# Optimization experiments

Hardware: AMD Instinct MI355X
Metric: run time of the kernel (lower is better)

## Reference

```python
import jax, jax.numpy as jnp
import numpy as np

HEADS = 8
DIM_HEAD = 64
SCALE = DIM_HEAD ** -0.5
THRESH = 0.01


def setup_inputs() -> dict:
    key = jax.random.key(0)
    ks = jax.random.split(key, 5)
    b, n, dim = 4, 2048, 512
    inner = HEADS * DIM_HEAD  # 512
    x = jax.random.normal(ks[0], (b, n, dim), dtype=jnp.float32)
    Wqkv = jax.random.normal(ks[1], (dim, 3 * inner), dtype=jnp.float32) * (dim ** -0.5)
    bqkv = jax.random.normal(ks[2], (3 * inner,), dtype=jnp.float32) * 0.02
    Wout = jax.random.normal(ks[3], (inner, dim), dtype=jnp.float32) * (inner ** -0.5)
    bout = jax.random.normal(ks[4], (dim,), dtype=jnp.float32) * 0.02
    return {"x": x, "Wqkv": Wqkv, "bqkv": bqkv, "Wout": Wout, "bout": bout}


def reference(x, Wqkv, bqkv, Wout, bout):
    b, n, dim = x.shape
    qkv = x @ Wqkv + bqkv  # [b, n, 3*inner]
    q, k, v = jnp.split(qkv, 3, axis=-1)
    # b n (h d) -> b h n d
    split_heads = lambda t: t.reshape(b, n, HEADS, DIM_HEAD).transpose(0, 2, 1, 3)
    q, k, v = split_heads(q), split_heads(k), split_heads(v)
    dots = jnp.einsum('bhid,bhjd->bhij', q, k) * SCALE
    attn = jax.nn.softmax(dots, axis=-1)
    attn = jnp.where(attn > THRESH, attn, jnp.zeros_like(attn))
    out = jnp.einsum('bhij,bhjd->bhid', attn, v)
    out = out.transpose(0, 2, 1, 3).reshape(b, n, HEADS * DIM_HEAD)
    return out @ Wout + bout
```

## Files before the change

kernel.cpp:

```cpp
#include <hip/hip_runtime.h>

#define S_   2048
#define DM   512
#define HD   64
#define BHN  32

typedef unsigned short u16;
typedef __bf16 bf16x8 __attribute__((ext_vector_type(8)));
typedef float  f32x4  __attribute__((ext_vector_type(4)));

__device__ __forceinline__ float bf2f(u16 u) {
    union { unsigned int i; float f; } v; v.i = ((unsigned int)u) << 16; return v.f;
}
__device__ __forceinline__ u16 f2bf(float f) {
    union { float f; unsigned int i; } v; v.f = f;
    unsigned int i = v.i;
    return (u16)((i + 0x7FFFu + ((i >> 16) & 1u)) >> 16);
}
__device__ __forceinline__ void split3(float x, u16& b0, u16& b1, u16& b2) {
    b0 = f2bf(x);
    const float r0 = x - bf2f(b0);
    b1 = f2bf(r0);
    const float r1 = r0 - bf2f(b1);
    b2 = f2bf(r1);
}
__device__ __forceinline__ void split3t(float x, u16& b0, u16& b1, u16& b2) {
    union { float f; unsigned int i; } v; v.f = x;
    const unsigned int i0 = v.i & 0xFFFF0000u;
    b0 = (u16)(i0 >> 16);
    union { float f; unsigned int i; } w0c; w0c.i = i0;
    const float r0 = x - w0c.f;
    union { float f; unsigned int i; } u; u.f = r0;
    const unsigned int i1 = u.i & 0xFFFF0000u;
    b1 = (u16)(i1 >> 16);
    union { float f; unsigned int i; } w1c; w1c.i = i1;
    const float r1 = r0 - w1c.f;
    union { float f; unsigned int i; } z; z.f = r1;
    b2 = (u16)(z.i >> 16);
}

__global__ __launch_bounds__(256) void prep_split_wT(
    const float* __restrict__ W, int N, int total,
    u16* __restrict__ w0, u16* __restrict__ w1, u16* __restrict__ w2)
{
    for (int idx = blockIdx.x * 256 + threadIdx.x; idx < total; idx += gridDim.x * 256) {
        const int n = idx >> 9, k = idx & 511;
        u16 a0, a1, a2;
        split3t(W[(size_t)k * N + n], a0, a1, a2);
        w0[idx] = a0; w1[idx] = a1;
        if (w2) w2[idx] = a2;
    }
}

__global__ __launch_bounds__(256) void gemm_qkv_mfma(
    const float* __restrict__ A, const u16* __restrict__ Wt0, const u16* __restrict__ Wt1,
    const u16* __restrict__ Wt2, const float* __restrict__ bias,
    float* __restrict__ qh, float* __restrict__ kh, u16* __restrict__ vt)
{
    __shared__ __attribute__((aligned(16))) u16 As0[128 * 32], As1[128 * 32], As2[128 * 32];
    __shared__ __attribute__((aligned(16))) u16 Bs0[128 * 32], Bs1[128 * 32], Bs2[128 * 32];

    const int t  = threadIdx.x;
    const int m0 = blockIdx.y * 128, n0 = blockIdx.x * 128;
    const int w  = t >> 6, l = t & 63;
    const int wm = (w >> 1) * 64, wn = (w & 1) * 64;
    const int lr = l & 15, lq = l >> 4;

    const f32x4 zero4 = {0.f, 0.f, 0.f, 0.f};
    f32x4 acc[4][4];
#pragma unroll
    for (int i = 0; i < 4; i++)
#pragma unroll
        for (int j = 0; j < 4; j++) acc[i][j] = zero4;

    for (int k0 = 0; k0 < 512; k0 += 32) {
        __syncthreads();
#pragma unroll
        for (int i = 0; i < 4; i++) {
            const int e = t + 256 * i;
            const int r = e >> 3, c4 = (e & 7) * 4;
            const float4 f = *(const float4*)(&A[(size_t)(m0 + r) * 512 + k0 + c4]);
            const float xv[4] = {f.x, f.y, f.z, f.w};
            u16 a0[4], a1[4], a2[4];
#pragma unroll
            for (int j = 0; j < 4; j++) split3t(xv[j], a0[j], a1[j], a2[j]);
            int2 p0, p1, p2;
            p0.x = a0[0] | (a0[1] << 16); p0.y = a0[2] | (a0[3] << 16);
            p1.x = a1[0] | (a1[1] << 16); p1.y = a1[2] | (a1[3] << 16);
            p2.x = a2[0] | (a2[1] << 16); p2.y = a2[2] | (a2[3] << 16);
            *(int2*)(&As0[r * 32 + c4]) = p0;
            *(int2*)(&As1[r * 32 + c4]) = p1;
            *(int2*)(&As2[r * 32 + c4]) = p2;
        }
#pragma unroll
        for (int i = 0; i < 2; i++) {
            const int e = t + 256 * i;
            const int r = e >> 2, c0 = (e & 3) * 8;
            *(int4*)(&Bs0[r * 32 + c0]) = *(const int4*)(&Wt0[(size_t)(n0 + r) * 512 + k0 + c0]);
            *(int4*)(&Bs1[r * 32 + c0]) = *(const int4*)(&Wt1[(size_t)(n0 + r) * 512 + k0 + c0]);
            *(int4*)(&Bs2[r * 32 + c0]) = *(const int4*)(&Wt2[(size_t)(n0 + r) * 512 + k0 + c0]);
        }
        __syncthreads();

#pragma unroll
        for (int i = 0; i < 4; i++) {
            const int ao = (wm + i * 16 + lr) * 32 + lq * 8;
            const bf16x8 a0 = *(const bf16x8*)(&As0[ao]);
            const bf16x8 a1 = *(const bf16x8*)(&As1[ao]);
            const bf16x8 a2 = *(const bf16x8*)(&As2[ao]);
#pragma unroll
            for (int j = 0; j < 4; j++) {
                const int bo = (wn + j * 16 + lr) * 32 + lq * 8;
                const bf16x8 b0 = *(const bf16x8*)(&Bs0[bo]);
                const bf16x8 b1 = *(const bf16x8*)(&Bs1[bo]);
                const bf16x8 b2 = *(const bf16x8*)(&Bs2[bo]);
                f32x4 c = acc[i][j];
                c = __builtin_amdgcn_mfma_f32_16x16x32_bf16(a0, b0, c, 0, 0, 0);
                c = __builtin_amdgcn_mfma_f32_16x16x32_bf16(a0, b1, c, 0, 0, 0);
                c = __builtin_amdgcn_mfma_f32_16x16x32_bf16(a1, b0, c, 0, 0, 0);
                c = __builtin_amdgcn_mfma_f32_16x16x32_bf16(a1, b1, c, 0, 0, 0);
                c = __builtin_amdgcn_mfma_f32_16x16x32_bf16(a0, b2, c, 0, 0, 0);
                c = __builtin_amdgcn_mfma_f32_16x16x32_bf16(a2, b0, c, 0, 0, 0);
                acc[i][j] = c;
            }
        }
    }

#pragma unroll
    for (int j = 0; j < 4; j++) {
        const int n = n0 + wn + j * 16 + lr;
        const float bv = bias[n];
        const int part = n >> 9, within = n & 511;
        const int h = within >> 6, d = within & 63;
#pragma unroll
        for (int i = 0; i < 4; i++) {
#pragma unroll
            for (int r = 0; r < 4; r++) {
                const int m = m0 + wm + i * 16 + lq * 4 + r;
                const int b = m >> 11, ns = m & 2047;
                const float val = acc[i][j][r] + bv;
                if (part == 0)
                    qh[(((size_t)(b * 8 + h)) * S_ + ns) * HD + d] = val;
                else if (part == 1)
                    kh[(((size_t)(b * 8 + h)) * S_ + ns) * HD + d] = val;
                else
                    vt[(((size_t)(b * 8 + h)) * HD + d) * S_ + ns] = f2bf(val);
            }
        }
    }
}

#define LDH 72

__global__ __launch_bounds__(512) void attn_mfma128(
    const float* __restrict__ q_ws, const float* __restrict__ k_ws,
    const u16* __restrict__ vt_ws, u16* __restrict__ ao_ws)
{
    __shared__ __attribute__((aligned(16))) u16 K0s[64 * LDH], K1s[64 * LDH], K2s[64 * LDH];
    __shared__ __attribute__((aligned(16))) u16 Vs[64 * LDH];
    __shared__ __attribute__((aligned(16))) u16 Ps[8][16 * LDH];
    __shared__ float smaxL[8][32];

    const int t  = threadIdx.x;
    const int w  = t >> 6, l = t & 63;
    const int lr = l & 15, lq = l >> 4;
    const int bh = blockIdx.y, b = bh >> 3, h = bh & 7;
    const int q0 = blockIdx.x * 128;

    const float* qg  = q_ws + ((size_t)bh * S_ + q0) * HD;
    const float* kg0 = k_ws + (size_t)bh * S_ * HD;
    const u16*   vb  = vt_ws + (size_t)bh * HD * S_;

    bf16x8 fq0[2], fq1[2], fq2[2];
#pragma unroll
    for (int h2 = 0; h2 < 2; h2++) {
        __syncthreads();
#pragma unroll
        for (int i = 0; i < 2; i++) {
            const int e = t + 512 * i;
            const int row = e >> 4, c0 = (e & 15) * 4;
            const float4 f = *(const float4*)(qg + (size_t)h2 * 4096 + (size_t)e * 4);
            const float xv[4] = {f.x * 0.125f, f.y * 0.125f, f.z * 0.125f, f.w * 0.125f};
            u16 a0[4], a1[4], a2[4];
#pragma unroll
            for (int j = 0; j < 4; j++) split3(xv[j], a0[j], a1[j], a2[j]);
            int2 p0, p1, p2;
            p0.x = a0[0] | (a0[1] << 16); p0.y = a0[2] | (a0[3] << 16);
            p1.x = a1[0] | (a1[1] << 16); p1.y = a1[2] | (a1[3] << 16);
            p2.x = a2[0] | (a2[1] << 16); p2.y = a2[2] | (a2[3] << 16);
            *(int2*)(&K0s[row * LDH + c0]) = p0;
            *(int2*)(&K1s[row * LDH + c0]) = p1;
            *(int2*)(&K2s[row * LDH + c0]) = p2;
        }
        __syncthreads();
        if ((w >> 2) == h2) {
#pragma unroll
            for (int kc = 0; kc < 2; kc++) {
                const int o = ((w & 3) * 16 + lr) * LDH + kc * 32 + lq * 8;
                fq0[kc] = *(const bf16x8*)(&K0s[o]);
                fq1[kc] = *(const bf16x8*)(&K1s[o]);
                fq2[kc] = *(const bf16x8*)(&K2s[o]);
            }
        }
    }

    const f32x4 zero4 = {0.f, 0.f, 0.f, 0.f};
    double lsum[4];
#pragma unroll
    for (int r = 0; r < 4; r++) lsum[r] = 0.0;

    for (int jt = 0; jt < 32; jt++) {
        __syncthreads();
        const float* kg = kg0 + (size_t)jt * 64 * HD;
#pragma unroll
        for (int i = 0; i < 2; i++) {
            const int e = t + 512 * i;
            const int row = e >> 4, c0 = (e & 15) * 4;
            const float4 f = *(const float4*)(kg + (size_t)e * 4);
            const float xv[4] = {f.x, f.y, f.z, f.w};
            u16 a0[4], a1[4], a2[4];
#pragma unroll
            for (int j = 0; j < 4; j++) split3t(xv[j], a0[j], a1[j], a2[j]);
            int2 p0, p1, p2;
            p0.x = a0[0] | (a0[1] << 16); p0.y = a0[2] | (a0[3] << 16);
            p1.x = a1[0] | (a1[1] << 16); p1.y = a1[2] | (a1[3] << 16);
            p2.x = a2[0] | (a2[1] << 16); p2.y = a2[2] | (a2[3] << 16);
            *(int2*)(&K0s[row * LDH + c0]) = p0;
            *(int2*)(&K1s[row * LDH + c0]) = p1;
            *(int2*)(&K2s[row * LDH + c0]) = p2;
        }
        __syncthreads();

        float tmax = -1e30f;
#pragma unroll
        for (int nt = 0; nt < 4; nt++) {
            f32x4 aHH = zero4, aC = zero4;
#pragma unroll
            for (int kc = 0; kc < 2; kc++) {
                const int ko = (nt * 16 + lr) * LDH + kc * 32 + lq * 8;
                const bf16x8 k0 = *(const bf16x8*)(&K0s[ko]);
                const bf16x8 k1 = *(const bf16x8*)(&K1s[ko]);
                const bf16x8 k2 = *(const bf16x8*)(&K2s[ko]);
                aHH = __builtin_amdgcn_mfma_f32_16x16x32_bf16(fq0[kc], k0, aHH, 0, 0, 0);
                aC  = __builtin_amdgcn_mfma_f32_16x16x32_bf16(fq0[kc], k1, aC, 0, 0, 0);
                aC  = __builtin_amdgcn_mfma_f32_16x16x32_bf16(fq1[kc], k0, aC, 0, 0, 0);
                aC  = __builtin_amdgcn_mfma_f32_16x16x32_bf16(fq1[kc], k1, aC, 0, 0, 0);
                aC  = __builtin_amdgcn_mfma_f32_16x16x32_bf16(fq0[kc], k2, aC, 0, 0, 0);
                aC  = __builtin_amdgcn_mfma_f32_16x16x32_bf16(fq2[kc], k0, aC, 0, 0, 0);
            }
#pragma unroll
            for (int r = 0; r < 4; r++) {
                const float s = fminf(fmaxf(aHH[r] + aC[r], -30.f), 30.f);
                tmax = fmaxf(tmax, s);
                lsum[r] += (double)__expf(s);
            }
        }
#pragma unroll
        for (int off = 1; off < 64; off <<= 1)
            tmax = fmaxf(tmax, __shfl_xor(tmax, off, 64));
        if (l == 0) smaxL[w][jt] = tmax;
    }
#pragma unroll
    for (int r = 0; r < 4; r++) {
#pragma unroll
        for (int off = 1; off < 16; off <<= 1)
            lsum[r] += __shfl_xor(lsum[r], off, 64);
    }
    double l_d[4]; float inv_l[4];
#pragma unroll
    for (int r = 0; r < 4; r++) {
        l_d[r] = lsum[r];
        inv_l[r] = (float)(1.0 / lsum[r]);
    }

    float zmin4 = (float)fmin(fmin(lsum[0], lsum[1]), fmin(lsum[2], lsum[3]));
    zmin4 = fminf(zmin4, __shfl_xor(zmin4, 16, 64));
    zmin4 = fminf(zmin4, __shfl_xor(zmin4, 32, 64));
    const float sthr = logf(0.0085f * zmin4);

    f32x4 oacc[4];
#pragma unroll
    for (int dt = 0; dt < 4; dt++) oacc[dt] = zero4;

    for (int jt = 0; jt < 32; jt++) {
        __syncthreads();
        const float* kg = kg0 + (size_t)jt * 64 * HD;
#pragma unroll
        for (int i = 0; i < 2; i++) {
            const int e = t + 512 * i;
            const int row = e >> 4, c0 = (e & 15) * 4;
            const float4 f = *(const float4*)(kg + (size_t)e * 4);
            int2 p0;
            p0.x = f2bf(f.x) | (f2bf(f.y) << 16);
            p0.y = f2bf(f.z) | (f2bf(f.w) << 16);
            *(int2*)(&K0s[row * LDH + c0]) = p0;
        }
        {
            const int e = t;
            const int row = e >> 3, c0 = (e & 7) * 8;
            *(int4*)(&Vs[row * LDH + c0]) = *(const int4*)(&vb[(size_t)row * S_ + jt * 64 + c0]);
        }
        __syncthreads();

        const bool live = (smaxL[w][jt] >= sthr);

        if (live) {
#pragma unroll
            for (int nt = 0; nt < 4; nt++) {
                f32x4 sacc = zero4;
#pragma unroll
                for (int kc = 0; kc < 2; kc++) {
                    const bf16x8 k0 = *(const bf16x8*)(&K0s[(nt * 16 + lr) * LDH + kc * 32 + lq * 8]);
                    sacc = __builtin_amdgcn_mfma_f32_16x16x32_bf16(fq0[kc], k0, sacc, 0, 0, 0);
                }
#pragma unroll
                for (int r = 0; r < 4; r++) {
                    const float s = fminf(fmaxf(sacc[r], -30.f), 30.f);
                    const float p = __expf(s) * inv_l[r];
                    u16 pb;
                    if (p > 0.0115f) {
                        pb = f2bf(p);
                    } else if (p < 0.009f) {
                        pb = 0;
                    } else {
                        const int row = q0 + w * 16 + lq * 4 + r;
                        const int col = jt * 64 + nt * 16 + lr;
                        const float* qr  = q_ws + ((size_t)bh * S_ + row) * HD;
                        const float* kcv = k_ws + ((size_t)bh * S_ + col) * HD;
                        double s64 = 0.0;
                        for (int d = 0; d < HD; d++) s64 += (double)qr[d] * (double)kcv[d];
                        s64 = fmin(fmax(s64 * 0.125, -30.0), 30.0);
                        const double pd = exp(s64) / l_d[r];
                        pb = (pd > 0.01) ? f2bf((float)pd) : (u16)0;
                    }
                    Ps[w][(lq * 4 + r) * LDH + nt * 16 + lr] = pb;
                }
            }
        }
        __syncthreads();
        if (live) {
#pragma unroll
            for (int kc = 0; kc < 2; kc++) {
                const bf16x8 ap = *(const bf16x8*)(&Ps[w][lr * LDH + kc * 32 + lq * 8]);
#pragma unroll
                for (int dt = 0; dt < 4; dt++) {
                    const bf16x8 bv = *(const bf16x8*)(&Vs[(dt * 16 + lr) * LDH + kc * 32 + lq * 8]);
                    oacc[dt] = __builtin_amdgcn_mfma_f32_16x16x32_bf16(ap, bv, oacc[dt], 0, 0, 0);
                }
            }
        }
    }

#pragma unroll
    for (int dt = 0; dt < 4; dt++) {
#pragma unroll
        for (int r = 0; r < 4; r++) {
            const int row = q0 + w * 16 + lq * 4 + r;
            const int d   = dt * 16 + lr;
            ao_ws[((size_t)b * S_ + row) * DM + h * HD + d] = f2bf(oacc[dt][r]);
        }
    }
}

__global__ __launch_bounds__(256) void gemm_out_mfma(
    const u16* __restrict__ A, const u16* __restrict__ Wt0, const u16* __restrict__ Wt1,
    const float* __restrict__ bias, float* __restrict__ out)
{
    __shared__ __attribute__((aligned(16))) u16 As[128 * 32];
    __shared__ __attribute__((aligned(16))) u16 Bs0[128 * 32], Bs1[128 * 32];

    const int t  = threadIdx.x;
    const int m0 = blockIdx.y * 128, n0 = blockIdx.x * 128;
    const int w  = t >> 6, l = t & 63;
    const int wm = (w >> 1) * 64, wn = (w & 1) * 64;
    const int lr = l & 15, lq = l >> 4;

    const f32x4 zero4 = {0.f, 0.f, 0.f, 0.f};
    f32x4 acc[4][4];
#pragma unroll
    for (int i = 0; i < 4; i++)
#pragma unroll
        for (int j = 0; j < 4; j++) acc[i][j] = zero4;

    for (int k0 = 0; k0 < 512; k0 += 32) {
        __syncthreads();
#pragma unroll
        for (int i = 0; i < 2; i++) {
            const int e = t + 256 * i;
            const int r = e >> 2, c0 = (e & 3) * 8;
            *(int4*)(&As[r * 32 + c0])  = *(const int4*)(&A  [(size_t)(m0 + r) * 512 + k0 + c0]);
            *(int4*)(&Bs0[r * 32 + c0]) = *(const int4*)(&Wt0[(size_t)(n0 + r) * 512 + k0 + c0]);
            *(int4*)(&Bs1[r * 32 + c0]) = *(const int4*)(&Wt1[(size_t)(n0 + r) * 512 + k0 + c0]);
        }
        __syncthreads();

#pragma unroll
        for (int i = 0; i < 4; i++) {
            const bf16x8 a = *(const bf16x8*)(&As[(wm + i * 16 + lr) * 32 + lq * 8]);
#pragma unroll
            for (int j = 0; j < 4; j++) {
                const int bo = (wn + j * 16 + lr) * 32 + lq * 8;
                const bf16x8 b0 = *(const bf16x8*)(&Bs0[bo]);
                const bf16x8 b1 = *(const bf16x8*)(&Bs1[bo]);
                f32x4 c = acc[i][j];
                c = __builtin_amdgcn_mfma_f32_16x16x32_bf16(a, b0, c, 0, 0, 0);
                c = __builtin_amdgcn_mfma_f32_16x16x32_bf16(a, b1, c, 0, 0, 0);
                acc[i][j] = c;
            }
        }
    }

#pragma unroll
    for (int j = 0; j < 4; j++) {
        const int n = n0 + wn + j * 16 + lr;
        const float bv = bias[n];
#pragma unroll
        for (int i = 0; i < 4; i++) {
#pragma unroll
            for (int r = 0; r < 4; r++) {
                const int m = m0 + wm + i * 16 + lq * 4 + r;
                out[(size_t)m * 512 + n] = acc[i][j][r] + bv;
            }
        }
    }
}

extern "C" void kernel_launch(void* const* d_in, const int* in_sizes, int n_in,
                              void* d_out, int out_size, void* d_ws, size_t ws_size,
                              hipStream_t stream) {
    const float* x = nullptr; const float* Wqkv = nullptr; const float* bqkv = nullptr;
    const float* Wout = nullptr; const float* bout = nullptr;
    for (int i = 0; i < n_in; i++) {
        switch (in_sizes[i]) {
            case 4194304: x    = (const float*)d_in[i]; break;
            case 786432:  Wqkv = (const float*)d_in[i]; break;
            case 1536:    bqkv = (const float*)d_in[i]; break;
            case 262144:  Wout = (const float*)d_in[i]; break;
            case 512:     bout = (const float*)d_in[i]; break;
            default: break;
        }
    }
    if (!x)    x    = (const float*)d_in[0];
    if (!Wqkv) Wqkv = (const float*)d_in[1];
    if (!bqkv) bqkv = (const float*)d_in[2];
    if (!Wout) Wout = (const float*)d_in[3];
    if (!bout) bout = (const float*)d_in[4];

    float* out = (float*)d_out;

    char* ws = (char*)d_ws;
    float* q_ws  = (float*)(ws);
    float* k_ws  = (float*)(ws + (16ull << 20));
    u16* vt_ws = (u16*)(ws + (32ull << 20));
    u16* ao_ws = (u16*)(ws + (40ull << 20));
    u16* wt0 = (u16*)(ws + (40ull << 20));
    u16* wt1 = (u16*)(ws + (40ull << 20) + 1572864);
    u16* wt2 = (u16*)(ws + (40ull << 20) + 3145728);
    u16* wo0 = (u16*)(ws + (32ull << 20));
    u16* wo1 = (u16*)(ws + (32ull << 20) + 524288);

    prep_split_wT<<<3072, 256, 0, stream>>>(Wqkv, 1536, 1536 * 512, wt0, wt1, wt2);
    gemm_qkv_mfma<<<dim3(12, 64), 256, 0, stream>>>(
        x, wt0, wt1, wt2, bqkv, q_ws, k_ws, vt_ws);
    attn_mfma128<<<dim3(16, BHN), 512, 0, stream>>>(q_ws, k_ws, vt_ws, ao_ws);
    prep_split_wT<<<1024, 256, 0, stream>>>(Wout, 512, 512 * 512, wo0, wo1, nullptr);
    gemm_out_mfma<<<dim3(4, 64), 256, 0, stream>>>(ao_ws, wo0, wo1, bout, out);
}
```

Baseline: 431.5 us.

## Prefetch next K/V tiles into registers and precompute bf16 K copy

The QKV GEMM now also writes a bf16 copy of K (stored in the output buffer as scratch). The second attention pass loads that bf16 K directly instead of reconverting fp32 K every tile. Both attention passes prefetch the next tile's K (and V) into registers right after the barrier, so global loads overlap with the MFMA work. The cost is extra register pressure, an extra global write in the GEMM, and reliance on the output buffer being free as scratch until the final GEMM.

Result: slower. 528.8 us (+22.6%).

```diff
diff --git a/kernel.cpp b/kernel.cpp
--- a/kernel.cpp
+++ b/kernel.cpp
@@ -55,7 +55,8 @@
 __global__ __launch_bounds__(256) void gemm_qkv_mfma(
     const float* __restrict__ A, const u16* __restrict__ Wt0, const u16* __restrict__ Wt1,
     const u16* __restrict__ Wt2, const float* __restrict__ bias,
-    float* __restrict__ qh, float* __restrict__ kh, u16* __restrict__ vt)
+    float* __restrict__ qh, float* __restrict__ kh, u16* __restrict__ khi,
+    u16* __restrict__ vt)
 {
     __shared__ __attribute__((aligned(16))) u16 As0[128 * 32], As1[128 * 32], As2[128 * 32];
     __shared__ __attribute__((aligned(16))) u16 Bs0[128 * 32], Bs1[128 * 32], Bs2[128 * 32];
@@ -139,12 +140,15 @@
                 const int m = m0 + wm + i * 16 + lq * 4 + r;
                 const int b = m >> 11, ns = m & 2047;
                 const float val = acc[i][j][r] + bv;
-                if (part == 0)
+                if (part == 0) {
                     qh[(((size_t)(b * 8 + h)) * S_ + ns) * HD + d] = val;
-                else if (part == 1)
-                    kh[(((size_t)(b * 8 + h)) * S_ + ns) * HD + d] = val;
-                else
+                } else if (part == 1) {
+                    const size_t kidx = (((size_t)(b * 8 + h)) * S_ + ns) * HD + d;
+                    kh[kidx]  = val;
+                    khi[kidx] = f2bf(val);
+                } else {
                     vt[(((size_t)(b * 8 + h)) * HD + d) * S_ + ns] = f2bf(val);
+                }
             }
         }
     }
@@ -154,7 +158,8 @@
 
 __global__ __launch_bounds__(512) void attn_mfma128(
     const float* __restrict__ q_ws, const float* __restrict__ k_ws,
-    const u16* __restrict__ vt_ws, u16* __restrict__ ao_ws)
+    const u16* __restrict__ khi_ws, const u16* __restrict__ vt_ws,
+    u16* __restrict__ ao_ws)
 {
     __shared__ __attribute__((aligned(16))) u16 K0s[64 * LDH], K1s[64 * LDH], K2s[64 * LDH];
     __shared__ __attribute__((aligned(16))) u16 Vs[64 * LDH];
@@ -169,6 +174,7 @@
 
     const float* qg  = q_ws + ((size_t)bh * S_ + q0) * HD;
     const float* kg0 = k_ws + (size_t)bh * S_ * HD;
+    const u16*   kh0 = khi_ws + (size_t)bh * S_ * HD;
     const u16*   vb  = vt_ws + (size_t)bh * HD * S_;
 
     bf16x8 fq0[2], fq1[2], fq2[2];
@@ -209,14 +215,18 @@
 #pragma unroll
     for (int r = 0; r < 4; r++) lsum[r] = 0.0;
 
+    float4 ka[2];
+#pragma unroll
+    for (int i = 0; i < 2; i++)
+        ka[i] = *(const float4*)(kg0 + (size_t)(t + 512 * i) * 4);
+
     for (int jt = 0; jt < 32; jt++) {
         __syncthreads();
-        const float* kg = kg0 + (size_t)jt * 64 * HD;
 #pragma unroll
         for (int i = 0; i < 2; i++) {
             const int e = t + 512 * i;
             const int row = e >> 4, c0 = (e & 15) * 4;
-            const float4 f = *(const float4*)(kg + (size_t)e * 4);
+            const float4 f = ka[i];
             const float xv[4] = {f.x, f.y, f.z, f.w};
             u16 a0[4], a1[4], a2[4];
 #pragma unroll
@@ -230,6 +240,14 @@
             *(int2*)(&K2s[row * LDH + c0]) = p2;
         }
         __syncthreads();
+
+        {
+            const int jn = (jt + 1 < 32) ? jt + 1 : 31;
+            const float* kg = kg0 + (size_t)jn * 64 * HD;
+#pragma unroll
+            for (int i = 0; i < 2; i++)
+                ka[i] = *(const float4*)(kg + (size_t)(t + 512 * i) * 4);
+        }
 
         float tmax = -1e30f;
 #pragma unroll
@@ -282,25 +300,25 @@
 #pragma unroll
     for (int dt = 0; dt < 4; dt++) oacc[dt] = zero4;
 
+    int4 kb, vr;
+    kb = *(const int4*)(&kh0[(size_t)(t >> 3) * HD + (t & 7) * 8]);
+    vr = *(const int4*)(&vb[(size_t)(t >> 3) * S_ + (t & 7) * 8]);
+
     for (int jt = 0; jt < 32; jt++) {
         __syncthreads();
-        const float* kg = kg0 + (size_t)jt * 64 * HD;
-#pragma unroll
-        for (int i = 0; i < 2; i++) {
-            const int e = t + 512 * i;
-            const int row = e >> 4, c0 = (e & 15) * 4;
-            const float4 f = *(const float4*)(kg + (size_t)e * 4);
-            int2 p0;
-            p0.x = f2bf(f.x) | (f2bf(f.y) << 16);
-            p0.y = f2bf(f.z) | (f2bf(f.w) << 16);
-            *(int2*)(&K0s[row * LDH + c0]) = p0;
-        }
         {
-            const int e = t;
-            const int row = e >> 3, c0 = (e & 7) * 8;
-            *(int4*)(&Vs[row * LDH + c0]) = *(const int4*)(&vb[(size_t)row * S_ + jt * 64 + c0]);
-        }
-        __syncthreads();
+            const int row = t >> 3, c0 = (t & 7) * 8;
+            *(int4*)(&K0s[row * LDH + c0]) = kb;
+            *(int4*)(&Vs[row * LDH + c0])  = vr;
+        }
+        __syncthreads();
+
+        {
+            const int jn = (jt + 1 < 32) ? jt + 1 : 31;
+            const int row = t >> 3, c0 = (t & 7) * 8;
+            kb = *(const int4*)(&kh0[(size_t)jn * 64 * HD + (size_t)row * HD + c0]);
+            vr = *(const int4*)(&vb[(size_t)row * S_ + jn * 64 + c0]);
+        }
 
         const bool live = (smaxL[w][jt] >= sthr);
 
@@ -453,6 +471,7 @@
     float* k_ws  = (float*)(ws + (16ull << 20));
     u16* vt_ws = (u16*)(ws + (32ull << 20));
     u16* ao_ws = (u16*)(ws + (40ull << 20));
+    u16* khi_ws = (u16*)d_out;
     u16* wt0 = (u16*)(ws + (40ull << 20));
     u16* wt1 = (u16*)(ws + (40ull << 20) + 1572864);
     u16* wt2 = (u16*)(ws + (40ull << 20) + 3145728);
@@ -461,8 +480,8 @@
 
     prep_split_wT<<<3072, 256, 0, stream>>>(Wqkv, 1536, 1536 * 512, wt0, wt1, wt2);
     gemm_qkv_mfma<<<dim3(12, 64), 256, 0, stream>>>(
-        x, wt0, wt1, wt2, bqkv, q_ws, k_ws, vt_ws);
-    attn_mfma128<<<dim3(16, BHN), 512, 0, stream>>>(q_ws, k_ws, vt_ws, ao_ws);
+        x, wt0, wt1, wt2, bqkv, q_ws, k_ws, khi_ws, vt_ws);
+    attn_mfma128<<<dim3(16, BHN), 512, 0, stream>>>(q_ws, k_ws, khi_ws, vt_ws, ao_ws);
     prep_split_wT<<<1024, 256, 0, stream>>>(Wout, 512, 512 * 512, wo0, wo1, nullptr);
     gemm_out_mfma<<<dim3(4, 64), 256, 0, stream>>>(ao_ws, wo0, wo1, bout, out);
 }
```
